# Kernel tuning notes

Hardware: AMD Instinct MI355X
Metric: run time of the kernel (lower is better)

The kernel has to match this reference:

```python
import jax, jax.numpy as jnp
import numpy as np
import math

N_HEADS = 16
EMBD = 1024
D_HEAD = EMBD // N_HEADS


def setup_inputs() -> dict:
    key = jax.random.key(0)
    ks = jax.random.split(key, 5)
    s = 1.0 / math.sqrt(EMBD)
    return {
        "x": jax.random.normal(ks[0], (2, 2048, EMBD), dtype=jnp.float32),
        "w_in": jax.random.normal(ks[1], (EMBD, 3 * EMBD), dtype=jnp.float32) * s,
        "b_in": jax.random.normal(ks[2], (3 * EMBD,), dtype=jnp.float32) * 0.02,
        "w_out": jax.random.normal(ks[3], (EMBD, EMBD), dtype=jnp.float32) * s,
        "b_out": jax.random.normal(ks[4], (EMBD,), dtype=jnp.float32) * 0.02,
    }


def reference(x, w_in, b_in, w_out, b_out):
    # x: [B, S, D]
    B, S, D = x.shape
    qkv = x @ w_in + b_in                      # [B, S, 3D]
    q, k, v = jnp.split(qkv, 3, axis=-1)
    # [B, S, H, dh] -> [B, H, S, dh]
    def heads(t):
        return t.reshape(B, S, N_HEADS, D_HEAD).transpose(0, 2, 1, 3)
    q, k, v = heads(q), heads(k), heads(v)
    scores = jnp.einsum("bhqd,bhkd->bhqk", q, k)  # [B, H, S, S]
    # causal mask applied before scaling (as in original; -inf invariant to scale)
    causal = jnp.tril(jnp.ones((S, S), dtype=bool))
    scores = jnp.where(causal, scores, -jnp.inf)
    scores = scores / jnp.asarray(math.sqrt(D_HEAD), dtype=scores.dtype)
    attn = jax.nn.softmax(scores, axis=-1)
    out = jnp.einsum("bhqk,bhkd->bhqd", attn, v)  # [B, H, S, dh]
    out = out.transpose(0, 2, 1, 3).reshape(B, S, D)
    return out @ w_out + b_out
```

## Files before the change

### kernel.cpp

```cpp
#include <hip/hip_runtime.h>
#include <stdint.h>

#define DEVI __device__ __forceinline__

typedef __attribute__((ext_vector_type(8))) short short8;
typedef __attribute__((ext_vector_type(4))) float f32x4;
typedef __attribute__((ext_vector_type(4))) uint32_t u32x4;

DEVI unsigned short f2bf(float f) {
    union { float f; uint32_t u; } v; v.f = f;
    return (unsigned short)((v.u + 0x7FFFu + ((v.u >> 16) & 1u)) >> 16);
}

DEVI uint32_t cvtpk_bf16(float a, float b) {
    uint32_t r;
    asm("v_cvt_pk_bf16_f32 %0, %1, %2" : "=v"(r) : "v"(a), "v"(b));
    return r;
}

DEVI void perm32(uint32_t &a, uint32_t &b) {
    asm("v_permlane32_swap_b32 %0, %1" : "+v"(a), "+v"(b));
}
DEVI void perm16(uint32_t &a, uint32_t &b) {
    asm("v_permlane16_swap_b32 %0, %1" : "+v"(a), "+v"(b));
}

DEVI void gload16(const void* g, void* l) {
    __builtin_amdgcn_global_load_lds(
        (const __attribute__((address_space(1))) unsigned int*)g,
        (__attribute__((address_space(3))) unsigned int*)l, 16, 0, 0);
}

__global__ void k_cvt(const float* __restrict__ in, ushort* __restrict__ out, int n4) {
    int i = blockIdx.x * blockDim.x + threadIdx.x;
    int stride = gridDim.x * blockDim.x;
    for (; i < n4; i += stride) {
        float4 v = ((const float4*)in)[i];
        ushort4 o;
        o.x = f2bf(v.x); o.y = f2bf(v.y); o.z = f2bf(v.z); o.w = f2bf(v.w);
        ((ushort4*)out)[i] = o;
    }
}

__global__ void k_tcvt(const float* __restrict__ in, ushort* __restrict__ out, int R, int C) {
    __shared__ float t[32][33];
    int c0 = blockIdx.x * 32, r0 = blockIdx.y * 32;
    int lr = threadIdx.x >> 5, lc = threadIdx.x & 31;
    #pragma unroll
    for (int i = 0; i < 4; i++)
        t[lr + 8*i][lc] = in[(size_t)(r0 + lr + 8*i)*C + c0 + lc];
    __syncthreads();
    #pragma unroll
    for (int i = 0; i < 4; i++)
        out[(size_t)(c0 + lr + 8*i)*R + r0 + lc] = f2bf(t[lc][lr + 8*i]);
}

template<int MODE>
__global__ __launch_bounds__(256, 2) void k_gemm(
    const ushort* __restrict__ A, const ushort* __restrict__ Bt,
    const float* __restrict__ bias,
    ushort* __restrict__ oQ, ushort* __restrict__ oK, ushort* __restrict__ oV,
    float* __restrict__ oF,
    int M, int N, int K, int S)
{
    __shared__ __align__(16) ushort As[128*64];
    __shared__ __align__(16) ushort Bs[128*64];
    const int tid = threadIdx.x;
    const int w = tid >> 6, l = tid & 63;

    int lin = blockIdx.y * gridDim.x + blockIdx.x;
    int nwg = gridDim.x * gridDim.y;
    int swz = (lin & 7) * (nwg >> 3) + (lin >> 3);
    const int m0 = (swz / gridDim.x) * 128, n0 = (swz % gridDim.x) * 128;

    const int wr = (w >> 1) * 64, wc = (w & 1) * 64;
    const int fr = l & 15, fg = l >> 4;
    const int lr8 = l >> 3;
    const int slot = (l & 7) ^ lr8;

    f32x4 acc[4][4] = {};

    const ushort* Abase = A + (size_t)(m0 + w*32 + lr8) * K + slot*8;
    const ushort* Bbase = Bt + (size_t)(n0 + w*32 + lr8) * K + slot*8;

    for (int k0 = 0; k0 < K; k0 += 64) {
        __syncthreads();
        #pragma unroll
        for (int i = 0; i < 4; i++) {
            gload16(Abase + (size_t)(8*i)*K + k0, &As[(w*32 + 8*i)*64]);
            gload16(Bbase + (size_t)(8*i)*K + k0, &Bs[(w*32 + 8*i)*64]);
        }
        __syncthreads();
        #pragma unroll
        for (int kk = 0; kk < 2; kk++) {
            short8 af[4], bfr[4];
            #pragma unroll
            for (int i = 0; i < 4; i++) {
                int ra = wr + i*16 + fr;
                af[i] = *(const short8*)((const char*)As + ra*128 + ((kk*64 + fg*16) ^ ((ra & 7) << 4)));
                int rb = wc + i*16 + fr;
                bfr[i] = *(const short8*)((const char*)Bs + rb*128 + ((kk*64 + fg*16) ^ ((rb & 7) << 4)));
            }
            #pragma unroll
            for (int i = 0; i < 4; i++)
                #pragma unroll
                for (int j = 0; j < 4; j++)
                    acc[i][j] = __builtin_amdgcn_mfma_f32_16x16x32_bf16(af[i], bfr[j], acc[i][j], 0, 0, 0);
        }
    }

    if (MODE == 1) {
        #pragma unroll
        for (int j = 0; j < 4; j++) {
            int n = n0 + wc + j*16 + fr;
            float bv = bias[n];
            #pragma unroll
            for (int i = 0; i < 4; i++) {
                int mrow = m0 + wr + i*16 + fg*4;
                #pragma unroll
                for (int r = 0; r < 4; r++)
                    oF[(size_t)(mrow + r)*N + n] = acc[i][j][r] + bv;
            }
        }
    } else {
        #pragma unroll
        for (int j = 0; j < 4; j++) {
            int n = n0 + wc + j*16 + fr;
            int region = n >> 10;
            int h = (n & 1023) >> 6;
            int d = n & 63;
            float bv = bias[n];
            float scl = (region == 0) ? 0.18033688011112042f : 1.0f;
            #pragma unroll
            for (int i = 0; i < 4; i++) {
                int mrow = m0 + wr + i*16 + fg*4;
                int b = mrow >> 11;
                int s = mrow & 2047;
                if (region < 2) {
                    ushort* dst = (region == 0 ? oQ : oK) + ((size_t)(b*16 + h)*S)*64 + (size_t)d;
                    #pragma unroll
                    for (int r = 0; r < 4; r++)
                        dst[(size_t)(s + r)*64] = f2bf((acc[i][j][r] + bv) * scl);
                } else {
                    ushort* dst = oV + ((size_t)(b*16 + h)*64 + d)*S + s;
                    ushort4 pk;
                    pk.x = f2bf(acc[i][j][0] + bv);
                    pk.y = f2bf(acc[i][j][1] + bv);
                    pk.z = f2bf(acc[i][j][2] + bv);
                    pk.w = f2bf(acc[i][j][3] + bv);
                    *(ushort4*)dst = pk;
                }
            }
        }
    }
}

__global__ __launch_bounds__(128, 2) void k_attn(
    const ushort* __restrict__ Q,
    const ushort* __restrict__ Kb,
    const ushort* __restrict__ Vt,
    float* __restrict__ po,
    float* __restrict__ pl,
    int S)
{
    __shared__ __align__(16) ushort Kt[2][64*64];

    const int tid = threadIdx.x, w = tid >> 6, l = tid & 63;
    const int bid = blockIdx.x;
    const int bh = bid & 31;
    const int c = (bid >> 5) & 1;
    const int qt = 31 - (bid >> 6);
    const int qw = qt * 64 + w * 32;
    const int fr = l & 15, fg = l >> 4;

    const int len0 = (qt + 2) >> 1;
    const int t0 = c ? len0 : 0;
    const int t1 = c ? (qt + 1) : len0;

    short8 qf[2][2];
    {
        const ushort* qp = Q + ((size_t)bh*S + qw + fr)*64 + fg*8;
        qf[0][0] = *(const short8*)(qp);
        qf[0][1] = *(const short8*)(qp + 32);
        qf[1][0] = *(const short8*)(qp + 16*64);
        qf[1][1] = *(const short8*)(qp + 16*64 + 32);
    }

    float l_[2] = {0.f, 0.f};
    f32x4 o_[2][4] = {};

    const int lr8 = l >> 3;
    const int slot = (l & 7) ^ lr8;
    const ushort* Ksrc = Kb + (size_t)bh*S*64;
    const ushort* Vsrc = Vt + (size_t)bh*64*S;

    auto stage = [&](int buf, int j0) {
        #pragma unroll
        for (int i = 0; i < 4; i++) {
            int rb = w*32 + i*8;
            gload16(Ksrc + (size_t)(j0 + rb + lr8)*64 + slot*8, &Kt[buf][rb*64]);
        }
    };

    if (t0 < t1) stage(0, t0 * 64);
    __syncthreads();
    int cur = 0;

    for (int jt = t0; jt < t1; jt++) {
        const int j0 = jt * 64;
        if (jt + 1 < t1) stage(cur ^ 1, j0 + 64);

        short8 vf[2][4];
        #pragma unroll
        for (int kk = 0; kk < 2; kk++)
            #pragma unroll
            for (int f = 0; f < 4; f++)
                vf[kk][f] = *(const short8*)(Vsrc + (size_t)(f*16 + fr)*S + j0 + kk*32 + fg*8);

        f32x4 sa[2][4] = {};
        __builtin_amdgcn_s_setprio(1);
        #pragma unroll
        for (int kk = 0; kk < 2; kk++) {
            short8 kf[4];
            #pragma unroll
            for (int f = 0; f < 4; f++) {
                int row = f*16 + fr;
                kf[f] = *(const short8*)((const char*)Kt[cur] + row*128 + ((kk*64 + fg*16) ^ ((row & 7) << 4)));
            }
            #pragma unroll
            for (int t = 0; t < 2; t++)
                #pragma unroll
                for (int f = 0; f < 4; f++)
                    sa[t][f] = __builtin_amdgcn_mfma_f32_16x16x32_bf16(kf[f], qf[t][kk], sa[t][f], 0, 0, 0);
        }
        __builtin_amdgcn_s_setprio(0);

        if (jt == qt) {
            #pragma unroll
            for (int t = 0; t < 2; t++) {
                int qg = qw + t*16 + fr;
                #pragma unroll
                for (int f = 0; f < 4; f++) {
                    int base = j0 + f*16 + fg*4 - qg;
                    #pragma unroll
                    for (int r = 0; r < 4; r++)
                        if (base + r > 0) sa[t][f][r] = -1e30f;
                }
            }
        }

        uint32_t cw[2][4][2];
        #pragma unroll
        for (int t = 0; t < 2; t++)
            #pragma unroll
            for (int f = 0; f < 4; f++) {
                float p0 = __builtin_amdgcn_exp2f(sa[t][f][0]);
                float p1 = __builtin_amdgcn_exp2f(sa[t][f][1]);
                float p2 = __builtin_amdgcn_exp2f(sa[t][f][2]);
                float p3 = __builtin_amdgcn_exp2f(sa[t][f][3]);
                l_[t] += (p0 + p1) + (p2 + p3);
                cw[t][f][0] = cvtpk_bf16(p0, p1);
                cw[t][f][1] = cvtpk_bf16(p2, p3);
            }

        __builtin_amdgcn_s_setprio(1);
        #pragma unroll
        for (int kk = 0; kk < 2; kk++) {
            short8 pf[2];
            #pragma unroll
            for (int t = 0; t < 2; t++) {
                uint32_t a0 = cw[t][2*kk][0], b0 = cw[t][2*kk + 1][0];
                perm32(a0, b0); perm16(a0, b0);
                uint32_t a1 = cw[t][2*kk][1], b1 = cw[t][2*kk + 1][1];
                perm32(a1, b1); perm16(a1, b1);
                u32x4 uw; uw[0] = a0; uw[1] = a1; uw[2] = b0; uw[3] = b1;
                pf[t] = __builtin_bit_cast(short8, uw);
            }
            #pragma unroll
            for (int f = 0; f < 4; f++)
                #pragma unroll
                for (int t = 0; t < 2; t++)
                    o_[t][f] = __builtin_amdgcn_mfma_f32_16x16x32_bf16(vf[kk][f], pf[t], o_[t][f], 0, 0, 0);
        }
        __builtin_amdgcn_s_setprio(0);

        __syncthreads();
        cur ^= 1;
    }

    #pragma unroll
    for (int t = 0; t < 2; t++) {
        l_[t] += __shfl_xor(l_[t], 16);
        l_[t] += __shfl_xor(l_[t], 32);
    }

    float* pob = po + ((size_t)bid * 2 + w) * 2048;
    #pragma unroll
    for (int t = 0; t < 2; t++) {
        #pragma unroll
        for (int f = 0; f < 4; f++)
            *(f32x4*)&pob[(((t*4 + f)*16 + fr)*4 + fg)*4] = o_[t][f];
        if (fg == 0) pl[(size_t)bid*64 + w*32 + t*16 + fr] = l_[t];
    }
}

__global__ __launch_bounds__(256) void k_comb(
    const float* __restrict__ po, const float* __restrict__ pl,
    ushort* __restrict__ O, int S)
{
    const int bx = blockIdx.x;
    const int qt = bx >> 5, bh = bx & 31;
    const int b = bh >> 4, h = bh & 15;
    const int iA = ((31 - qt) << 6) | bh;
    const int iB = iA | 32;
    const f32x4* pa = (const f32x4*)(po + (size_t)iA * 4096);
    const f32x4* pb = (const f32x4*)(po + (size_t)iB * 4096);
    const float* la = pl + (size_t)iA * 64;
    const float* lb = pl + (size_t)iB * 64;

    #pragma unroll
    for (int k = 0; k < 4; k++) {
        int ss = threadIdx.x + 256 * k;
        int w = (ss >> 9) & 1, t = (ss >> 8) & 1, f = (ss >> 6) & 3, fr = (ss >> 2) & 15, fg = ss & 3;
        int row = w*32 + t*16 + fr;
        f32x4 a = pa[ss], c = pb[ss];
        float den = fmaxf(la[row] + lb[row], 1e-30f);
        float inv = 1.0f / den;
        ushort4 pk;
        pk.x = f2bf((a[0] + c[0]) * inv);
        pk.y = f2bf((a[1] + c[1]) * inv);
        pk.z = f2bf((a[2] + c[2]) * inv);
        pk.w = f2bf((a[3] + c[3]) * inv);
        int q = qt*64 + row;
        *(ushort4*)&O[((size_t)(b*S + q))*1024 + h*64 + f*16 + fg*4] = pk;
    }
}

extern "C" void kernel_launch(void* const* d_in, const int* in_sizes, int n_in,
                              void* d_out, int out_size, void* d_ws, size_t ws_size,
                              hipStream_t stream)
{
    const float* x     = (const float*)d_in[0];
    const float* w_in  = (const float*)d_in[1];
    const float* b_in  = (const float*)d_in[2];
    const float* w_out = (const float*)d_in[3];
    const float* b_out = (const float*)d_in[4];
    float* out = (float*)d_out;

    const int B = 2, S = 2048, D = 1024, H = 16;
    const int M = B * S;

    if (ws_size < (80u << 20)) return;
    char* ws = (char*)d_ws;
    ushort* xb     = (ushort*)(ws);
    ushort* w_inT  = (ushort*)(ws + (8u << 20));
    ushort* w_outT = (ushort*)(ws + (14u << 20));
    ushort* qb     = (ushort*)(ws + (16u << 20));
    ushort* kb     = (ushort*)(ws + (24u << 20));
    ushort* vtb    = (ushort*)(ws + (32u << 20));
    float*  po     = (float*)(ws + (40u << 20));
    float*  pl     = (float*)(ws + (75u << 20));

    k_cvt<<<2048, 256, 0, stream>>>(x, xb, M*D/4);
    k_tcvt<<<dim3(3*D/32, D/32), 256, 0, stream>>>(w_in, w_inT, D, 3*D);
    k_tcvt<<<dim3(D/32, D/32), 256, 0, stream>>>(w_out, w_outT, D, D);
    k_gemm<0><<<dim3(3*D/128, M/128), 256, 0, stream>>>(xb, w_inT, b_in, qb, kb, vtb, nullptr, M, 3*D, D, S);
    k_attn<<<2048, 128, 0, stream>>>(qb, kb, vtb, po, pl, S);
    k_comb<<<1024, 256, 0, stream>>>(po, pl, xb, S);
    k_gemm<1><<<dim3(D/128, M/128), 256, 0, stream>>>(xb, w_outT, b_out, nullptr, nullptr, nullptr, out, M, D, D, S);
}
```

Measured before the change: 120.4 us.

## Split attention into single-wave blocks reading K directly from global memory

Each attention block becomes one 64-lane wave instead of two, so the grid doubles to 4096 blocks, and output indices are remapped so the combine kernel sees the same partial layout. The LDS double-buffered K staging and its __syncthreads are removed, and K fragments are loaded straight from global memory (through cache) into registers. V loads are moved next to the PV MFMAs. The aim is to remove barrier and LDS overhead and to raise occupancy. In exchange, the two waves sharing a q-tile no longer share K, so more global/L2 traffic is likely, and the K load latency is no longer hidden by prefetch.

```diff
diff --git a/kernel.cpp b/kernel.cpp
--- a/kernel.cpp
+++ b/kernel.cpp
@@ -155,7 +155,7 @@
     }
 }
 
-__global__ __launch_bounds__(128, 2) void k_attn(
+__global__ __launch_bounds__(64, 3) void k_attn(
     const ushort* __restrict__ Q,
     const ushort* __restrict__ Kb,
     const ushort* __restrict__ Vt,
@@ -163,15 +163,16 @@
     float* __restrict__ pl,
     int S)
 {
-    __shared__ __align__(16) ushort Kt[2][64*64];
-
-    const int tid = threadIdx.x, w = tid >> 6, l = tid & 63;
+    const int l = threadIdx.x;
     const int bid = blockIdx.x;
     const int bh = bid & 31;
-    const int c = (bid >> 5) & 1;
-    const int qt = 31 - (bid >> 6);
+    const int w = (bid >> 5) & 1;
+    const int qtc = bid >> 6;
+    const int c = qtc & 1;
+    const int qt = 31 - (qtc >> 1);
     const int qw = qt * 64 + w * 32;
     const int fr = l & 15, fg = l >> 4;
+    const int obid = ((31 - qt) << 6) | (c << 5) | bh;
 
     const int len0 = (qt + 2) >> 1;
     const int t0 = c ? len0 : 0;
@@ -189,50 +190,28 @@
     float l_[2] = {0.f, 0.f};
     f32x4 o_[2][4] = {};
 
-    const int lr8 = l >> 3;
-    const int slot = (l & 7) ^ lr8;
-    const ushort* Ksrc = Kb + (size_t)bh*S*64;
-    const ushort* Vsrc = Vt + (size_t)bh*64*S;
-
-    auto stage = [&](int buf, int j0) {
-        #pragma unroll
-        for (int i = 0; i < 4; i++) {
-            int rb = w*32 + i*8;
-            gload16(Ksrc + (size_t)(j0 + rb + lr8)*64 + slot*8, &Kt[buf][rb*64]);
-        }
-    };
-
-    if (t0 < t1) stage(0, t0 * 64);
-    __syncthreads();
-    int cur = 0;
+    const ushort* Ksrc = Kb + (size_t)bh*S*64 + (size_t)fr*64 + fg*8;
+    const ushort* Vsrc = Vt + (size_t)bh*64*S + (size_t)fr*S + fg*8;
 
     for (int jt = t0; jt < t1; jt++) {
         const int j0 = jt * 64;
-        if (jt + 1 < t1) stage(cur ^ 1, j0 + 64);
-
-        short8 vf[2][4];
+
+        short8 kf[2][4];
         #pragma unroll
         for (int kk = 0; kk < 2; kk++)
             #pragma unroll
             for (int f = 0; f < 4; f++)
-                vf[kk][f] = *(const short8*)(Vsrc + (size_t)(f*16 + fr)*S + j0 + kk*32 + fg*8);
+                kf[kk][f] = *(const short8*)(Ksrc + (size_t)(j0 + f*16)*64 + kk*32);
 
         f32x4 sa[2][4] = {};
         __builtin_amdgcn_s_setprio(1);
         #pragma unroll
-        for (int kk = 0; kk < 2; kk++) {
-            short8 kf[4];
-            #pragma unroll
-            for (int f = 0; f < 4; f++) {
-                int row = f*16 + fr;
-                kf[f] = *(const short8*)((const char*)Kt[cur] + row*128 + ((kk*64 + fg*16) ^ ((row & 7) << 4)));
-            }
+        for (int kk = 0; kk < 2; kk++)
             #pragma unroll
             for (int t = 0; t < 2; t++)
                 #pragma unroll
                 for (int f = 0; f < 4; f++)
-                    sa[t][f] = __builtin_amdgcn_mfma_f32_16x16x32_bf16(kf[f], qf[t][kk], sa[t][f], 0, 0, 0);
-        }
+                    sa[t][f] = __builtin_amdgcn_mfma_f32_16x16x32_bf16(kf[kk][f], qf[t][kk], sa[t][f], 0, 0, 0);
         __builtin_amdgcn_s_setprio(0);
 
         if (jt == qt) {
@@ -263,9 +242,12 @@
                 cw[t][f][1] = cvtpk_bf16(p2, p3);
             }
 
-        __builtin_amdgcn_s_setprio(1);
         #pragma unroll
         for (int kk = 0; kk < 2; kk++) {
+            short8 vf[4];
+            #pragma unroll
+            for (int f = 0; f < 4; f++)
+                vf[f] = *(const short8*)(Vsrc + (size_t)(f*16)*S + j0 + kk*32);
             short8 pf[2];
             #pragma unroll
             for (int t = 0; t < 2; t++) {
@@ -276,16 +258,14 @@
                 u32x4 uw; uw[0] = a0; uw[1] = a1; uw[2] = b0; uw[3] = b1;
                 pf[t] = __builtin_bit_cast(short8, uw);
             }
+            __builtin_amdgcn_s_setprio(1);
             #pragma unroll
             for (int f = 0; f < 4; f++)
                 #pragma unroll
                 for (int t = 0; t < 2; t++)
-                    o_[t][f] = __builtin_amdgcn_mfma_f32_16x16x32_bf16(vf[kk][f], pf[t], o_[t][f], 0, 0, 0);
-        }
-        __builtin_amdgcn_s_setprio(0);
-
-        __syncthreads();
-        cur ^= 1;
+                    o_[t][f] = __builtin_amdgcn_mfma_f32_16x16x32_bf16(vf[f], pf[t], o_[t][f], 0, 0, 0);
+            __builtin_amdgcn_s_setprio(0);
+        }
     }
 
     #pragma unroll
@@ -294,13 +274,13 @@
         l_[t] += __shfl_xor(l_[t], 32);
     }
 
-    float* pob = po + ((size_t)bid * 2 + w) * 2048;
+    float* pob = po + ((size_t)obid * 2 + w) * 2048;
     #pragma unroll
     for (int t = 0; t < 2; t++) {
         #pragma unroll
         for (int f = 0; f < 4; f++)
             *(f32x4*)&pob[(((t*4 + f)*16 + fr)*4 + fg)*4] = o_[t][f];
-        if (fg == 0) pl[(size_t)bid*64 + w*32 + t*16 + fr] = l_[t];
+        if (fg == 0) pl[(size_t)obid*64 + w*32 + t*16 + fr] = l_[t];
     }
 }
 
@@ -365,7 +345,7 @@
     k_tcvt<<<dim3(3*D/32, D/32), 256, 0, stream>>>(w_in, w_inT, D, 3*D);
     k_tcvt<<<dim3(D/32, D/32), 256, 0, stream>>>(w_out, w_outT, D, D);
     k_gemm<0><<<dim3(3*D/128, M/128), 256, 0, stream>>>(xb, w_inT, b_in, qb, kb, vtb, nullptr, M, 3*D, D, S);
-    k_attn<<<2048, 128, 0, stream>>>(qb, kb, vtb, po, pl, S);
+    k_attn<<<4096, 64, 0, stream>>>(qb, kb, vtb, po, pl, S);
     k_comb<<<1024, 256, 0, stream>>>(po, pl, xb, S);
     k_gemm<1><<<dim3(D/128, M/128), 256, 0, stream>>>(xb, w_outT, b_out, nullptr, nullptr, nullptr, out, M, D, D, S);
 }
```

Measured after the change: 143.4 us. +19.1%, slower.
